# Optimization experiments

Hardware: AMD Instinct MI355X
Metric: run time of the kernel (lower is better)

The kernel has to match this reference:

```python
import jax, jax.numpy as jnp
import numpy as np
import math

B, S, D = 2, 4096, 512
H, DH = 8, 64
L = 128            # num_landmarks
W = 128            # window_size
EXT = W // 2       # 64
WIN = 2 * EXT + W  # 256
G = S // W         # 32 chunks
EPS = 1e-5


def _ln(x, g, b):
    mu = jnp.mean(x, axis=-1, keepdims=True)
    var = jnp.mean((x - mu) ** 2, axis=-1, keepdims=True)
    return (x - mu) * jax.lax.rsqrt(var + EPS) * g + b


def setup_inputs() -> dict:
    key = jax.random.key(0)
    ks = jax.random.split(key, 12)
    sd = 1.0 / math.sqrt(D)
    inp = {
        "X": jax.random.normal(ks[0], (B, S, D), dtype=jnp.float32),
        "mask": jnp.ones((B, S), dtype=jnp.int32),
        "Wq": jax.random.normal(ks[1], (D, H * DH), dtype=jnp.float32) * sd,
        "bq": jnp.zeros((H * DH,), jnp.float32),
        "Wk": jax.random.normal(ks[2], (D, H * DH), dtype=jnp.float32) * sd,
        "bk": jnp.zeros((H * DH,), jnp.float32),
        "Wv": jax.random.normal(ks[3], (D, H * DH), dtype=jnp.float32) * sd,
        "bv": jnp.zeros((H * DH,), jnp.float32),
        "Wo": jax.random.normal(ks[4], (H * DH, D), dtype=jnp.float32) * sd,
        "bo": jnp.zeros((D,), jnp.float32),
        "ln_l_g": jnp.ones((H * DH,), jnp.float32),
        "ln_l_b": jnp.zeros((H * DH,), jnp.float32),
        "ln_s_g": jnp.ones((H * DH,), jnp.float32),
        "ln_s_b": jnp.zeros((H * DH,), jnp.float32),
        "Wd": jax.random.normal(ks[5], (D, H * L), dtype=jnp.float32) * sd,
        "bd": jnp.zeros((H * L,), jnp.float32),
    }
    return inp


def reference(X, mask, Wq, bq, Wk, bk, Wv, bv, Wo, bo,
              ln_l_g, ln_l_b, ln_s_g, ln_s_b, Wd, bd):
    scale = 1.0 / math.sqrt(DH)

    def split(x):  # [B,S,H*DH] -> [B,H,S,DH]
        return x.reshape(B, S, H, DH).transpose(0, 2, 1, 3)

    Q = split(X @ Wq + bq) * scale
    K = split(_ln(X @ Wk + bk, ln_l_g, ln_l_b))
    V = split(_ln(X @ Wv + bv, ln_l_g, ln_l_b))
    pad_mask = (mask == 0)  # True = padding, [B,S]

    # ---- landmark compression branch ----
    hs = jax.nn.softmax((X @ Wd + bd).astype(jnp.float32), axis=1)  # over seq
    hs = hs.astype(X.dtype).reshape(B, S, H, L).transpose(0, 2, 3, 1)  # [B,H,L,S]
    Kc = jnp.einsum('bhls,bhsd->bhld', hs, K)
    Vc = jnp.einsum('bhls,bhsd->bhld', hs, V)
    # dual_ln_s over full model dim
    Kc = _ln(Kc.transpose(0, 2, 1, 3).reshape(B, L, H * DH), ln_s_g, ln_s_b)
    Kc = Kc.reshape(B, L, H, DH).transpose(0, 2, 1, 3)
    Vc = _ln(Vc.transpose(0, 2, 1, 3).reshape(B, L, H * DH), ln_s_g, ln_s_b)
    Vc = Vc.reshape(B, L, H, DH).transpose(0, 2, 1, 3)

    attn_c = jnp.einsum('bhqd,bhld->bhql', Q, Kc)  # [B,H,S,L]

    # ---- sliding-window branch (v2 tiling) ----
    idx = jnp.arange(G)[:, None] * W + jnp.arange(WIN)[None, :]
    K_pad = jnp.pad(K, ((0, 0), (0, 0), (EXT, EXT), (0, 0)))
    K_tiles = K_pad[:, :, idx, :]
    Qt = Q.reshape(B, H, G, W, DH)
    win_scores = jnp.einsum('bhgqd,bhgkd->bhgqk', Qt, K_tiles)
    mask_pad = jnp.pad(pad_mask, ((0, 0), (EXT, EXT)), constant_values=True)
    mask_tiles = mask_pad[:, idx]
    win_scores = jnp.where(mask_tiles[:, None, :, None, :], -jnp.inf, win_scores)
    win_scores = win_scores.reshape(B, H, S, WIN)

    # ---- joint softmax over [landmarks | window] ----
    all_scores = jnp.concatenate([attn_c, win_scores], axis=-1)
    all_attn = jax.nn.softmax(all_scores.astype(jnp.float32), axis=-1).astype(X.dtype)
    all_attn = jnp.where(pad_mask[:, None, :, None], 0.0, all_attn)

    C = jnp.einsum('bhql,bhld->bhqd', all_attn[..., :L], Vc)
    wp = all_attn[..., L:].reshape(B, H, G, W, WIN)
    V_pad = jnp.pad(V, ((0, 0), (0, 0), (EXT, EXT), (0, 0)))
    V_tiles = V_pad[:, :, idx, :]
    C = C + jnp.einsum('bhgqk,bhgkd->bhgqd', wp, V_tiles).reshape(B, H, S, DH)

    out = C.transpose(0, 2, 1, 3).reshape(B, S, H * DH) @ Wo + bo
    return out
```

## Files before the change

### kernel.cpp

```cpp
#include <hip/hip_runtime.h>
#include <hip/hip_bf16.h>

#define S_LEN 4096
#define Hn 8
#define DHn 64
#define Lc 128
#define HL 1024
#define KD 512

typedef __attribute__((ext_vector_type(8))) short bshort8;
typedef __attribute__((ext_vector_type(4))) float f32x4;

__device__ __forceinline__ short f2bs(float f) {
    union { float f; unsigned u; } x; x.f = f;
    const unsigned r = x.u + 0x7FFFu + ((x.u >> 16) & 1u);
    return (short)(r >> 16);
}
__device__ __forceinline__ float bs2f(short s) {
    union { unsigned u; float f; } x; x.u = ((unsigned)(unsigned short)s) << 16;
    return x.f;
}

__device__ __forceinline__ void gl16(const short* g, short* l) {
    __builtin_amdgcn_global_load_lds((const __attribute__((address_space(1))) void*)g,
                                     (__attribute__((address_space(3))) void*)l, 16, 0, 0);
}

__global__ __launch_bounds__(256) void prep_all(const float* __restrict__ X,
    const float* __restrict__ Wq, const float* __restrict__ Wk, const float* __restrict__ Wv,
    const float* __restrict__ Wd, const float* __restrict__ Wo,
    short* __restrict__ Xbf, short* __restrict__ WTall, short* __restrict__ WoT)
{
    const int t = threadIdx.x;
    int blk = blockIdx.x;
    if (blk < 2048) {
        const int i = (blk * 256 + t) * 8;
        const float4 a = *(const float4*)&X[i];
        const float4 b = *(const float4*)&X[i + 4];
        bshort8 o;
        o[0] = f2bs(a.x); o[1] = f2bs(a.y); o[2] = f2bs(a.z); o[3] = f2bs(a.w);
        o[4] = f2bs(b.x); o[5] = f2bs(b.y); o[6] = f2bs(b.z); o[7] = f2bs(b.w);
        *(bshort8*)&Xbf[i] = o;
        return;
    }
    blk -= 2048;
    const float* W; short* out; int N;
    if (blk < 256)       { W = Wq; out = WTall;              N = 512;  }
    else if (blk < 512)  { W = Wk; out = WTall + 512 * 512;  N = 512;  blk -= 256; }
    else if (blk < 768)  { W = Wv; out = WTall + 1024 * 512; N = 512;  blk -= 512; }
    else if (blk < 1280) { W = Wd; out = WTall + 1536 * 512; N = 1024; blk -= 768; }
    else                 { W = Wo; out = WoT;                N = 512;  blk -= 1280; }
    const int nb = N >> 5;
    const int n0 = (blk % nb) * 32, k0 = (blk / nb) * 32;
    __shared__ float Tl[32][33];
    const int tx = t & 31, ty = t >> 5;
#pragma unroll
    for (int i = ty; i < 32; i += 8)
        Tl[i][tx] = W[(size_t)(k0 + i) * N + n0 + tx];
    __syncthreads();
#pragma unroll
    for (int i = ty; i < 32; i += 8)
        out[(size_t)(n0 + i) * KD + k0 + tx] = f2bs(Tl[tx][i]);
}

__global__ __launch_bounds__(256) void gemm_proj(const short* __restrict__ Xbf,
    const short* __restrict__ WT,
    const float* __restrict__ bq, const float* __restrict__ bk,
    const float* __restrict__ bv, const float* __restrict__ bd,
    short* __restrict__ Qbf, short* __restrict__ KbBf, short* __restrict__ VbBf,
    short* __restrict__ DlogBf)
{
    __shared__ __align__(16) short A_s[128 * 64];
    __shared__ __align__(16) short B_s[128 * 64];
    const int t = threadIdx.x;
    const int n0 = blockIdx.x * 128, m0 = blockIdx.y * 128;
    const int lane = t & 63, wave = t >> 6;
    const int wm = wave >> 1, wn = wave & 1;
    const int quad = lane >> 4, r15 = lane & 15;
    const int srow = t >> 3, scol = (t & 7) * 8;
    f32x4 acc[4][4];
#pragma unroll
    for (int i = 0; i < 4; ++i)
#pragma unroll
        for (int j = 0; j < 4; ++j) acc[i][j] = (f32x4){0.f, 0.f, 0.f, 0.f};

    for (int kk = 0; kk < KD; kk += 64) {
#pragma unroll
        for (int r = 0; r < 4; ++r) {
            gl16(&Xbf[(size_t)(m0 + r * 32 + srow) * KD + kk + scol], &A_s[r * 2048 + t * 8]);
            gl16(&WT[(size_t)(n0 + r * 32 + srow) * KD + kk + scol],  &B_s[r * 2048 + t * 8]);
        }
        __syncthreads();
#pragma unroll
        for (int ks = 0; ks < 2; ++ks) {
            bshort8 af[4], bfr[4];
#pragma unroll
            for (int i = 0; i < 4; ++i) af[i]  = *(const bshort8*)&A_s[(wm * 64 + i * 16 + r15) * 64 + ks * 32 + quad * 8];
#pragma unroll
            for (int j = 0; j < 4; ++j) bfr[j] = *(const bshort8*)&B_s[(wn * 64 + j * 16 + r15) * 64 + ks * 32 + quad * 8];
#pragma unroll
            for (int i = 0; i < 4; ++i)
#pragma unroll
                for (int j = 0; j < 4; ++j)
                    acc[i][j] = __builtin_amdgcn_mfma_f32_16x16x32_bf16(af[i], bfr[j], acc[i][j], 0, 0, 0);
        }
        __syncthreads();
    }
    const int seg = (n0 >= 1536) ? 3 : (n0 >> 9);
#pragma unroll
    for (int i = 0; i < 4; ++i)
#pragma unroll
        for (int j = 0; j < 4; ++j)
#pragma unroll
            for (int r = 0; r < 4; ++r) {
                const int gm = m0 + wm * 64 + i * 16 + quad * 4 + r;
                const int gn = n0 + wn * 64 + j * 16 + r15;
                float v = acc[i][j][r];
                if (seg == 0) {
                    v = (v + bq[gn]) * 0.125f;
                    const int bb = gm >> 12, s = gm & 4095, hh = gn >> 6, d = gn & 63;
                    Qbf[((size_t)(bb * Hn + hh) * S_LEN + s) * DHn + d] = f2bs(v);
                } else if (seg == 1) {
                    KbBf[(size_t)gm * 512 + (gn - 512)] = f2bs(v + bk[gn - 512]);
                } else if (seg == 2) {
                    VbBf[(size_t)gm * 512 + (gn - 1024)] = f2bs(v + bv[gn - 1024]);
                } else {
                    DlogBf[(size_t)gm * 1024 + (gn - 1536)] = f2bs(v + bd[gn - 1536]);
                }
            }
}

__global__ __launch_bounds__(256) void gemm_out(const short* __restrict__ Abf,
    const short* __restrict__ WT, const float* __restrict__ bias, float* __restrict__ outp)
{
    __shared__ __align__(16) short A_s[64 * 32];
    __shared__ __align__(16) short B_s[64 * 32];
    const int t = threadIdx.x;
    const int n0 = blockIdx.x * 64, m0 = blockIdx.y * 64;
    const int lane = t & 63, wave = t >> 6;
    const int quad = lane >> 4, r15 = lane & 15;
    const int eOff = t * 8;
    const int am = eOff >> 5, ak = eOff & 31;
    f32x4 acc[4];
#pragma unroll
    for (int j = 0; j < 4; ++j) acc[j] = (f32x4){0.f, 0.f, 0.f, 0.f};

    for (int kk = 0; kk < KD; kk += 32) {
        gl16(&Abf[(size_t)(m0 + am) * KD + kk + ak], &A_s[eOff]);
        gl16(&WT[(size_t)(n0 + am) * KD + kk + ak],  &B_s[eOff]);
        __syncthreads();
        const bshort8 af = *(const bshort8*)&A_s[(wave * 16 + r15) * 32 + quad * 8];
#pragma unroll
        for (int j = 0; j < 4; ++j) {
            const bshort8 bfr = *(const bshort8*)&B_s[(j * 16 + r15) * 32 + quad * 8];
            acc[j] = __builtin_amdgcn_mfma_f32_16x16x32_bf16(af, bfr, acc[j], 0, 0, 0);
        }
        __syncthreads();
    }
#pragma unroll
    for (int j = 0; j < 4; ++j)
#pragma unroll
        for (int r = 0; r < 4; ++r) {
            const int gm = m0 + wave * 16 + quad * 4 + r;
            const int gn = n0 + j * 16 + r15;
            outp[(size_t)gm * 512 + gn] = acc[j][r] + bias[gn];
        }
}

__global__ __launch_bounds__(256) void ln_ip(const short* __restrict__ KbBf, const short* __restrict__ VbBf,
    const float* __restrict__ g, const float* __restrict__ beta,
    short* __restrict__ Kbf, short* __restrict__ Vbf)
{
    const short* src = blockIdx.y ? VbBf : KbBf;
    short* dst = blockIdx.y ? Vbf : Kbf;
    const int row = blockIdx.x, t = threadIdx.x;
    const size_t base = (size_t)row * 512;
    const float x0 = bs2f(src[base + t]);
    const float x1 = bs2f(src[base + t + 256]);
    float s = x0 + x1, ss = x0 * x0 + x1 * x1;
#pragma unroll
    for (int off = 32; off >= 1; off >>= 1) { s += __shfl_xor(s, off); ss += __shfl_xor(ss, off); }
    __shared__ float red[2][4];
    if ((t & 63) == 0) { red[0][t >> 6] = s; red[1][t >> 6] = ss; }
    __syncthreads();
    s = red[0][0] + red[0][1] + red[0][2] + red[0][3];
    ss = red[1][0] + red[1][1] + red[1][2] + red[1][3];
    const float mu = s * (1.f / 512.f);
    const float r = rsqrtf(ss * (1.f / 512.f) - mu * mu + 1e-5f);
    const int bb = row >> 12, sidx = row & 4095;
#pragma unroll
    for (int half = 0; half < 2; ++half) {
        const int c = t + half * 256;
        const float x = half ? x1 : x0;
        const float v = (x - mu) * r * g[c] + beta[c];
        dst[((size_t)(bb * Hn + (c >> 6)) * S_LEN + sidx) * DHn + (c & 63)] = f2bs(v);
    }
}

__global__ __launch_bounds__(256) void kcvc_mfma(const short* __restrict__ Dlog,
    const short* __restrict__ Kbf, const short* __restrict__ Vbf,
    short* __restrict__ partK, short* __restrict__ partV, float* __restrict__ partZ)
{
    __shared__ __align__(16) short aa[128 * 72];
    __shared__ __align__(16) short Kt[64 * 72];
    __shared__ __align__(16) short Vt[64 * 72];
    __shared__ float zsh[256];
    const int t = threadIdx.x;
    const int seg = blockIdx.x, h = blockIdx.y, b = blockIdx.z;
    const int s0 = seg * 128;
    const size_t bh = (size_t)(b * Hn + h);
    const int lane = t & 63, wave = t >> 6;
    const int quad = lane >> 4, r15 = lane & 15;
    const int al = t & 127, ah = t >> 7;
    const int vj = t & 63, vd0 = (t >> 6) * 16;
    float zacc = 0.f;
    f32x4 aK[2][4], aV[2][4];
#pragma unroll
    for (int i = 0; i < 2; ++i)
#pragma unroll
        for (int j = 0; j < 4; ++j) { aK[i][j] = (f32x4){0.f,0.f,0.f,0.f}; aV[i][j] = (f32x4){0.f,0.f,0.f,0.f}; }

    for (int c = 0; c < 2; ++c) {
        const int sc0 = s0 + c * 64;
        if (c) __syncthreads();
#pragma unroll
        for (int gch = 0; gch < 4; ++gch) {
            bshort8 o;
#pragma unroll
            for (int j = 0; j < 8; ++j) {
                const int s = sc0 + ah * 32 + gch * 8 + j;
                const float e = __expf(bs2f(Dlog[((size_t)b * S_LEN + s) * HL + h * Lc + al]));
                zacc += e;
                o[j] = f2bs(e);
            }
            *(bshort8*)&aa[al * 72 + ah * 32 + gch * 8] = o;
        }
        {
            const size_t rb = (bh * S_LEN + sc0 + vj) * DHn + vd0;
            const bshort8 k0 = *(const bshort8*)&Kbf[rb];
            const bshort8 k1 = *(const bshort8*)&Kbf[rb + 8];
            const bshort8 v0 = *(const bshort8*)&Vbf[rb];
            const bshort8 v1 = *(const bshort8*)&Vbf[rb + 8];
#pragma unroll
            for (int i = 0; i < 8; ++i) {
                Kt[(vd0 + i) * 72 + vj] = k0[i]; Kt[(vd0 + 8 + i) * 72 + vj] = k1[i];
                Vt[(vd0 + i) * 72 + vj] = v0[i]; Vt[(vd0 + 8 + i) * 72 + vj] = v1[i];
            }
        }
        __syncthreads();
#pragma unroll
        for (int ks = 0; ks < 2; ++ks) {
            const bshort8 a0 = *(const bshort8*)&aa[(wave * 32 + r15) * 72 + ks * 32 + quad * 8];
            const bshort8 a1 = *(const bshort8*)&aa[(wave * 32 + 16 + r15) * 72 + ks * 32 + quad * 8];
#pragma unroll
            for (int j = 0; j < 4; ++j) {
                const bshort8 bk = *(const bshort8*)&Kt[(j * 16 + r15) * 72 + ks * 32 + quad * 8];
                const bshort8 bv = *(const bshort8*)&Vt[(j * 16 + r15) * 72 + ks * 32 + quad * 8];
                aK[0][j] = __builtin_amdgcn_mfma_f32_16x16x32_bf16(a0, bk, aK[0][j], 0, 0, 0);
                aK[1][j] = __builtin_amdgcn_mfma_f32_16x16x32_bf16(a1, bk, aK[1][j], 0, 0, 0);
                aV[0][j] = __builtin_amdgcn_mfma_f32_16x16x32_bf16(a0, bv, aV[0][j], 0, 0, 0);
                aV[1][j] = __builtin_amdgcn_mfma_f32_16x16x32_bf16(a1, bv, aV[1][j], 0, 0, 0);
            }
        }
    }
    zsh[t] = zacc;
    __syncthreads();
    if (t < 128)
        partZ[((size_t)(bh * Lc + t)) * 32 + seg] = zsh[t] + zsh[t + 128];
#pragma unroll
    for (int i = 0; i < 2; ++i)
#pragma unroll
        for (int j = 0; j < 4; ++j)
#pragma unroll
            for (int r = 0; r < 4; ++r) {
                const int l = wave * 32 + i * 16 + quad * 4 + r;
                const int d = j * 16 + r15;
                const size_t o = (((size_t)(b * Lc + l)) * 32 + seg) * 512 + h * 64 + d;
                partK[o] = f2bs(aK[i][j][r]);
                partV[o] = f2bs(aV[i][j][r]);
            }
}

__global__ __launch_bounds__(256) void kcvc_s2(const short* __restrict__ partK,
    const short* __restrict__ partV, const float* __restrict__ partZ,
    const float* __restrict__ g, const float* __restrict__ beta,
    short* __restrict__ KcBf, short* __restrict__ VcBf)
{
    const int l = blockIdx.x, b = blockIdx.y, t = threadIdx.x;
    __shared__ float zh[8];
    if (t < 8) {
        float z = 0.f;
        const size_t zb = ((size_t)((b * Hn + t) * Lc + l)) * 32;
#pragma unroll
        for (int seg = 0; seg < 32; ++seg) z += partZ[zb + seg];
        zh[t] = 1.f / z;
    }
    const size_t base = ((size_t)(b * Lc + l)) * 32 * 512;
    float k0 = 0.f, k1 = 0.f, v0 = 0.f, v1 = 0.f;
    for (int ch = 0; ch < 32; ++ch) {
        const size_t o = base + (size_t)ch * 512;
        k0 += bs2f(partK[o + t]);       k1 += bs2f(partK[o + t + 256]);
        v0 += bs2f(partV[o + t]);       v1 += bs2f(partV[o + t + 256]);
    }
    __syncthreads();
    const float z0 = zh[t >> 6], z1 = zh[(t + 256) >> 6];
    k0 *= z0; k1 *= z1; v0 *= z0; v1 *= z1;
    float sk = k0 + k1, ssk = k0 * k0 + k1 * k1;
    float sv = v0 + v1, ssv = v0 * v0 + v1 * v1;
#pragma unroll
    for (int off = 32; off >= 1; off >>= 1) {
        sk += __shfl_xor(sk, off); ssk += __shfl_xor(ssk, off);
        sv += __shfl_xor(sv, off); ssv += __shfl_xor(ssv, off);
    }
    __shared__ float red[4][4];
    if ((t & 63) == 0) {
        red[0][t >> 6] = sk; red[1][t >> 6] = ssk;
        red[2][t >> 6] = sv; red[3][t >> 6] = ssv;
    }
    __syncthreads();
    sk = red[0][0] + red[0][1] + red[0][2] + red[0][3];
    ssk = red[1][0] + red[1][1] + red[1][2] + red[1][3];
    sv = red[2][0] + red[2][1] + red[2][2] + red[2][3];
    ssv = red[3][0] + red[3][1] + red[3][2] + red[3][3];
    const float muK = sk * (1.f / 512.f);
    const float rK = rsqrtf(ssk * (1.f / 512.f) - muK * muK + 1e-5f);
    const float muV = sv * (1.f / 512.f);
    const float rV = rsqrtf(ssv * (1.f / 512.f) - muV * muV + 1e-5f);
#pragma unroll
    for (int half = 0; half < 2; ++half) {
        const int c = t + half * 256;
        const float xk = half ? k1 : k0;
        const float xv = half ? v1 : v0;
        const size_t o = ((size_t)(b * Hn + (c >> 6)) * Lc + l) * DHn + (c & 63);
        KcBf[o] = f2bs((xk - muK) * rK * g[c] + beta[c]);
        VcBf[o] = f2bs((xv - muV) * rV * g[c] + beta[c]);
    }
}

__global__ __launch_bounds__(256) void attn_mfma(
    const short* __restrict__ Qbf, const short* __restrict__ Kbf, const short* __restrict__ Vbf,
    const short* __restrict__ KcBf, const short* __restrict__ VcBf,
    const int* __restrict__ mask, short* __restrict__ C)
{
    __shared__ __align__(16) short Q_l[64 * 72];
    __shared__ __align__(16) short K_l[64 * 72];
    __shared__ __align__(16) short Vt_l[64 * 72];
    __shared__ __align__(16) short P_l[64 * 72];
    __shared__ float vb[64];
    const int t = threadIdx.x;
    const int qt = blockIdx.x, h = blockIdx.y, b = blockIdx.z;
    const int q0 = qt * 64, gg = qt >> 1;
    const size_t bh = (size_t)(b * Hn + h);
    const int lane = t & 63, wave = t >> 6;
    const int quad = lane >> 4, r15 = lane & 15;
    const int sr = t >> 2, sc = (t & 3) * 16;
    const int vj = t & 63, vd0 = (t >> 6) * 16;

    {
        const size_t gq = (bh * S_LEN + q0 + sr) * DHn + sc;
        const bshort8 a = *(const bshort8*)&Qbf[gq];
        const bshort8 b8 = *(const bshort8*)&Qbf[gq + 8];
        *(bshort8*)&Q_l[sr * 72 + sc] = a;
        *(bshort8*)&Q_l[sr * 72 + sc + 8] = b8;
    }
    f32x4 o[4];
#pragma unroll
    for (int df = 0; df < 4; ++df) o[df] = (f32x4){0.f, 0.f, 0.f, 0.f};
    float lrow[4] = {0.f, 0.f, 0.f, 0.f};

    for (int cc = 0; cc < 6; ++cc) {
        const short* ksrc; const short* vsrc;
        int sk0 = 0;
        if (cc < 2) {
            ksrc = &KcBf[(bh * Lc + cc * 64) * DHn];
            vsrc = &VcBf[(bh * Lc + cc * 64) * DHn];
        } else {
            sk0 = gg * 128 - 64 + (cc - 2) * 64;
            if (sk0 < 0 || sk0 >= S_LEN) continue;
            ksrc = &Kbf[(bh * S_LEN + sk0) * DHn];
            vsrc = &Vbf[(bh * S_LEN + sk0) * DHn];
        }
        __syncthreads();
        if (t < 64) {
            float v = 0.f;
            if (cc >= 2 && mask[b * S_LEN + sk0 + t] == 0) v = -1e30f;
            vb[t] = v;
        }
        {
            const bshort8 a = *(const bshort8*)&ksrc[sr * 64 + sc];
            const bshort8 b8 = *(const bshort8*)&ksrc[sr * 64 + sc + 8];
            *(bshort8*)&K_l[sr * 72 + sc] = a;
            *(bshort8*)&K_l[sr * 72 + sc + 8] = b8;
        }
        {
            const bshort8 v0 = *(const bshort8*)&vsrc[vj * 64 + vd0];
            const bshort8 v1 = *(const bshort8*)&vsrc[vj * 64 + vd0 + 8];
#pragma unroll
            for (int i = 0; i < 8; ++i) {
                Vt_l[(vd0 + i) * 72 + vj] = v0[i];
                Vt_l[(vd0 + 8 + i) * 72 + vj] = v1[i];
            }
        }
        __syncthreads();
        f32x4 c[4];
#pragma unroll
        for (int jf = 0; jf < 4; ++jf) c[jf] = (f32x4){0.f, 0.f, 0.f, 0.f};
#pragma unroll
        for (int ks = 0; ks < 2; ++ks) {
            const bshort8 aq = *(const bshort8*)&Q_l[(wave * 16 + r15) * 72 + ks * 32 + quad * 8];
#pragma unroll
            for (int jf = 0; jf < 4; ++jf) {
                const bshort8 bk = *(const bshort8*)&K_l[(jf * 16 + r15) * 72 + ks * 32 + quad * 8];
                c[jf] = __builtin_amdgcn_mfma_f32_16x16x32_bf16(aq, bk, c[jf], 0, 0, 0);
            }
        }
        float vbl[4];
#pragma unroll
        for (int jf = 0; jf < 4; ++jf) vbl[jf] = vb[jf * 16 + r15];
        float sum[4] = {0.f, 0.f, 0.f, 0.f};
#pragma unroll
        for (int jf = 0; jf < 4; ++jf)
#pragma unroll
            for (int r = 0; r < 4; ++r) {
                const float p = __expf(c[jf][r] + vbl[jf]);
                sum[r] += p;
                P_l[(wave * 16 + quad * 4 + r) * 72 + jf * 16 + r15] = f2bs(p);
            }
#pragma unroll
        for (int off = 1; off <= 8; off <<= 1)
#pragma unroll
            for (int r = 0; r < 4; ++r) sum[r] += __shfl_xor(sum[r], off);
#pragma unroll
        for (int r = 0; r < 4; ++r) lrow[r] += sum[r];
#pragma unroll
        for (int ks = 0; ks < 2; ++ks) {
            const bshort8 ap = *(const bshort8*)&P_l[(wave * 16 + r15) * 72 + ks * 32 + quad * 8];
#pragma unroll
            for (int df = 0; df < 4; ++df) {
                const bshort8 bv = *(const bshort8*)&Vt_l[(df * 16 + r15) * 72 + ks * 32 + quad * 8];
                o[df] = __builtin_amdgcn_mfma_f32_16x16x32_bf16(ap, bv, o[df], 0, 0, 0);
            }
        }
    }
#pragma unroll
    for (int r = 0; r < 4; ++r) {
        const int q = q0 + wave * 16 + quad * 4 + r;
        const float rl = (mask[b * S_LEN + q] == 0) ? 0.f : (1.f / lrow[r]);
        const size_t ob = ((size_t)b * S_LEN + q) * 512 + h * 64;
#pragma unroll
        for (int df = 0; df < 4; ++df)
            C[ob + df * 16 + r15] = f2bs(o[df][r] * rl);
    }
}

extern "C" void kernel_launch(void* const* d_in, const int* in_sizes, int n_in,
                              void* d_out, int out_size, void* d_ws, size_t ws_size,
                              hipStream_t stream) {
    (void)in_sizes; (void)n_in; (void)out_size; (void)ws_size;
    const float* X    = (const float*)d_in[0];
    const int*   mask = (const int*)d_in[1];
    const float* Wq = (const float*)d_in[2];  const float* bq = (const float*)d_in[3];
    const float* Wk = (const float*)d_in[4];  const float* bk = (const float*)d_in[5];
    const float* Wv = (const float*)d_in[6];  const float* bv = (const float*)d_in[7];
    const float* Wo = (const float*)d_in[8];  const float* bo = (const float*)d_in[9];
    const float* lnlg = (const float*)d_in[10]; const float* lnlb = (const float*)d_in[11];
    const float* lnsg = (const float*)d_in[12]; const float* lnsb = (const float*)d_in[13];
    const float* Wd = (const float*)d_in[14]; const float* bd = (const float*)d_in[15];

    short* sw = (short*)d_ws;
    short* Qbf    = sw;
    short* Kbf    = Qbf + 4194304;
    short* Vbf    = Kbf + 4194304;
    short* KbBf   = Vbf + 4194304;
    short* VbBf   = KbBf + 4194304;
    short* DlogBf = VbBf + 4194304;
    short* Xbf    = DlogBf + 8388608;
    short* WTall  = Xbf + 4194304;
    short* WoT    = WTall + 1310720;
    short* KcBf   = WoT + 262144;
    short* VcBf   = KcBf + 131072;
    short* partV  = VcBf + 131072;
    float* partZ  = (float*)(partV + 4194304);
    short* partK  = Xbf;
    short* Cbf    = Xbf;

    const dim3 blk(256);
    prep_all<<<3584, blk, 0, stream>>>(X, Wq, Wk, Wv, Wd, Wo, Xbf, WTall, WoT);
    gemm_proj<<<dim3(20, 64), blk, 0, stream>>>(Xbf, WTall, bq, bk, bv, bd, Qbf, KbBf, VbBf, DlogBf);
    ln_ip<<<dim3(8192, 2), blk, 0, stream>>>(KbBf, VbBf, lnlg, lnlb, Kbf, Vbf);
    kcvc_mfma<<<dim3(32, 8, 2), blk, 0, stream>>>(DlogBf, Kbf, Vbf, partK, partV, partZ);
    kcvc_s2<<<dim3(128, 2), blk, 0, stream>>>(partK, partV, partZ, lnsg, lnsb, KcBf, VcBf);
    attn_mfma<<<dim3(64, 8, 2), blk, 0, stream>>>(Qbf, Kbf, Vbf, KcBf, VcBf, mask, Cbf);
    gemm_out<<<dim3(8, 128), blk, 0, stream>>>(Cbf, WoT, bo, (float*)d_out);
}
```

Baseline: 238.3 us.

## Double attention query tile to 128 rows and halve projection GEMM K-step

```diff
diff --git a/kernel.cpp b/kernel.cpp
--- a/kernel.cpp
+++ b/kernel.cpp
@@ -70,40 +70,37 @@
     short* __restrict__ Qbf, short* __restrict__ KbBf, short* __restrict__ VbBf,
     short* __restrict__ DlogBf)
 {
-    __shared__ __align__(16) short A_s[128 * 64];
-    __shared__ __align__(16) short B_s[128 * 64];
+    __shared__ __align__(16) short A_s[128 * 32];
+    __shared__ __align__(16) short B_s[128 * 32];
     const int t = threadIdx.x;
     const int n0 = blockIdx.x * 128, m0 = blockIdx.y * 128;
     const int lane = t & 63, wave = t >> 6;
     const int wm = wave >> 1, wn = wave & 1;
     const int quad = lane >> 4, r15 = lane & 15;
-    const int srow = t >> 3, scol = (t & 7) * 8;
+    const int eOff = t * 8;
+    const int am = eOff >> 5, ak = eOff & 31;
     f32x4 acc[4][4];
 #pragma unroll
     for (int i = 0; i < 4; ++i)
 #pragma unroll
         for (int j = 0; j < 4; ++j) acc[i][j] = (f32x4){0.f, 0.f, 0.f, 0.f};
 
-    for (int kk = 0; kk < KD; kk += 64) {
-#pragma unroll
-        for (int r = 0; r < 4; ++r) {
-            gl16(&Xbf[(size_t)(m0 + r * 32 + srow) * KD + kk + scol], &A_s[r * 2048 + t * 8]);
-            gl16(&WT[(size_t)(n0 + r * 32 + srow) * KD + kk + scol],  &B_s[r * 2048 + t * 8]);
-        }
-        __syncthreads();
-#pragma unroll
-        for (int ks = 0; ks < 2; ++ks) {
-            bshort8 af[4], bfr[4];
-#pragma unroll
-            for (int i = 0; i < 4; ++i) af[i]  = *(const bshort8*)&A_s[(wm * 64 + i * 16 + r15) * 64 + ks * 32 + quad * 8];
-#pragma unroll
-            for (int j = 0; j < 4; ++j) bfr[j] = *(const bshort8*)&B_s[(wn * 64 + j * 16 + r15) * 64 + ks * 32 + quad * 8];
-#pragma unroll
-            for (int i = 0; i < 4; ++i)
-#pragma unroll
-                for (int j = 0; j < 4; ++j)
-                    acc[i][j] = __builtin_amdgcn_mfma_f32_16x16x32_bf16(af[i], bfr[j], acc[i][j], 0, 0, 0);
-        }
+    for (int kk = 0; kk < KD; kk += 32) {
+        gl16(&Xbf[(size_t)(m0 + am) * KD + kk + ak],      &A_s[eOff]);
+        gl16(&Xbf[(size_t)(m0 + 64 + am) * KD + kk + ak], &A_s[2048 + eOff]);
+        gl16(&WT[(size_t)(n0 + am) * KD + kk + ak],       &B_s[eOff]);
+        gl16(&WT[(size_t)(n0 + 64 + am) * KD + kk + ak],  &B_s[2048 + eOff]);
+        __syncthreads();
+        bshort8 af[4], bfr[4];
+#pragma unroll
+        for (int i = 0; i < 4; ++i) af[i]  = *(const bshort8*)&A_s[(wm * 64 + i * 16 + r15) * 32 + quad * 8];
+#pragma unroll
+        for (int j = 0; j < 4; ++j) bfr[j] = *(const bshort8*)&B_s[(wn * 64 + j * 16 + r15) * 32 + quad * 8];
+#pragma unroll
+        for (int i = 0; i < 4; ++i)
+#pragma unroll
+            for (int j = 0; j < 4; ++j)
+                acc[i][j] = __builtin_amdgcn_mfma_f32_16x16x32_bf16(af[i], bfr[j], acc[i][j], 0, 0, 0);
         __syncthreads();
     }
     const int seg = (n0 >= 1536) ? 3 : (n0 >> 9);
@@ -342,31 +339,35 @@
     const short* __restrict__ KcBf, const short* __restrict__ VcBf,
     const int* __restrict__ mask, short* __restrict__ C)
 {
-    __shared__ __align__(16) short Q_l[64 * 72];
+    __shared__ __align__(16) short Q_l[128 * 72];
     __shared__ __align__(16) short K_l[64 * 72];
     __shared__ __align__(16) short Vt_l[64 * 72];
-    __shared__ __align__(16) short P_l[64 * 72];
+    __shared__ __align__(16) short P_l[128 * 72];
     __shared__ float vb[64];
     const int t = threadIdx.x;
     const int qt = blockIdx.x, h = blockIdx.y, b = blockIdx.z;
-    const int q0 = qt * 64, gg = qt >> 1;
+    const int q0 = qt * 128;
     const size_t bh = (size_t)(b * Hn + h);
     const int lane = t & 63, wave = t >> 6;
     const int quad = lane >> 4, r15 = lane & 15;
     const int sr = t >> 2, sc = (t & 3) * 16;
     const int vj = t & 63, vd0 = (t >> 6) * 16;
 
-    {
-        const size_t gq = (bh * S_LEN + q0 + sr) * DHn + sc;
+#pragma unroll
+    for (int r = 0; r < 2; ++r) {
+        const int row = r * 64 + sr;
+        const size_t gq = (bh * S_LEN + q0 + row) * DHn + sc;
         const bshort8 a = *(const bshort8*)&Qbf[gq];
         const bshort8 b8 = *(const bshort8*)&Qbf[gq + 8];
-        *(bshort8*)&Q_l[sr * 72 + sc] = a;
-        *(bshort8*)&Q_l[sr * 72 + sc + 8] = b8;
-    }
-    f32x4 o[4];
-#pragma unroll
-    for (int df = 0; df < 4; ++df) o[df] = (f32x4){0.f, 0.f, 0.f, 0.f};
-    float lrow[4] = {0.f, 0.f, 0.f, 0.f};
+        *(bshort8*)&Q_l[row * 72 + sc] = a;
+        *(bshort8*)&Q_l[row * 72 + sc + 8] = b8;
+    }
+    f32x4 o[2][4];
+#pragma unroll
+    for (int i = 0; i < 2; ++i)
+#pragma unroll
+        for (int df = 0; df < 4; ++df) o[i][df] = (f32x4){0.f, 0.f, 0.f, 0.f};
+    float lrow[2][4] = {{0.f, 0.f, 0.f, 0.f}, {0.f, 0.f, 0.f, 0.f}};
 
     for (int cc = 0; cc < 6; ++cc) {
         const short* ksrc; const short* vsrc;
@@ -375,7 +376,7 @@
             ksrc = &KcBf[(bh * Lc + cc * 64) * DHn];
             vsrc = &VcBf[(bh * Lc + cc * 64) * DHn];
         } else {
-            sk0 = gg * 128 - 64 + (cc - 2) * 64;
+            sk0 = q0 - 64 + (cc - 2) * 64;
             if (sk0 < 0 || sk0 >= S_LEN) continue;
             ksrc = &Kbf[(bh * S_LEN + sk0) * DHn];
             vsrc = &Vbf[(bh * S_LEN + sk0) * DHn];
@@ -402,55 +403,73 @@
             }
         }
         __syncthreads();
-        f32x4 c[4];
-#pragma unroll
-        for (int jf = 0; jf < 4; ++jf) c[jf] = (f32x4){0.f, 0.f, 0.f, 0.f};
+        f32x4 c[2][4];
+#pragma unroll
+        for (int i = 0; i < 2; ++i)
+#pragma unroll
+            for (int jf = 0; jf < 4; ++jf) c[i][jf] = (f32x4){0.f, 0.f, 0.f, 0.f};
 #pragma unroll
         for (int ks = 0; ks < 2; ++ks) {
-            const bshort8 aq = *(const bshort8*)&Q_l[(wave * 16 + r15) * 72 + ks * 32 + quad * 8];
+            bshort8 aq[2];
+#pragma unroll
+            for (int i = 0; i < 2; ++i)
+                aq[i] = *(const bshort8*)&Q_l[(wave * 32 + i * 16 + r15) * 72 + ks * 32 + quad * 8];
 #pragma unroll
             for (int jf = 0; jf < 4; ++jf) {
                 const bshort8 bk = *(const bshort8*)&K_l[(jf * 16 + r15) * 72 + ks * 32 + quad * 8];
-                c[jf] = __builtin_amdgcn_mfma_f32_16x16x32_bf16(aq, bk, c[jf], 0, 0, 0);
+                c[0][jf] = __builtin_amdgcn_mfma_f32_16x16x32_bf16(aq[0], bk, c[0][jf], 0, 0, 0);
+                c[1][jf] = __builtin_amdgcn_mfma_f32_16x16x32_bf16(aq[1], bk, c[1][jf], 0, 0, 0);
             }
         }
         float vbl[4];
 #pragma unroll
         for (int jf = 0; jf < 4; ++jf) vbl[jf] = vb[jf * 16 + r15];
-        float sum[4] = {0.f, 0.f, 0.f, 0.f};
-#pragma unroll
-        for (int jf = 0; jf < 4; ++jf)
-#pragma unroll
-            for (int r = 0; r < 4; ++r) {
-                const float p = __expf(c[jf][r] + vbl[jf]);
-                sum[r] += p;
-                P_l[(wave * 16 + quad * 4 + r) * 72 + jf * 16 + r15] = f2bs(p);
-            }
+        float sum[2][4] = {{0.f, 0.f, 0.f, 0.f}, {0.f, 0.f, 0.f, 0.f}};
+#pragma unroll
+        for (int i = 0; i < 2; ++i)
+#pragma unroll
+            for (int jf = 0; jf < 4; ++jf)
+#pragma unroll
+                for (int r = 0; r < 4; ++r) {
+                    const float p = __expf(c[i][jf][r] + vbl[jf]);
+                    sum[i][r] += p;
+                    P_l[(wave * 32 + i * 16 + quad * 4 + r) * 72 + jf * 16 + r15] = f2bs(p);
+                }
 #pragma unroll
         for (int off = 1; off <= 8; off <<= 1)
 #pragma unroll
-            for (int r = 0; r < 4; ++r) sum[r] += __shfl_xor(sum[r], off);
-#pragma unroll
-        for (int r = 0; r < 4; ++r) lrow[r] += sum[r];
+            for (int i = 0; i < 2; ++i)
+#pragma unroll
+                for (int r = 0; r < 4; ++r) sum[i][r] += __shfl_xor(sum[i][r], off);
+#pragma unroll
+        for (int i = 0; i < 2; ++i)
+#pragma unroll
+            for (int r = 0; r < 4; ++r) lrow[i][r] += sum[i][r];
 #pragma unroll
         for (int ks = 0; ks < 2; ++ks) {
-            const bshort8 ap = *(const bshort8*)&P_l[(wave * 16 + r15) * 72 + ks * 32 + quad * 8];
+            bshort8 ap[2];
+#pragma unroll
+            for (int i = 0; i < 2; ++i)
+                ap[i] = *(const bshort8*)&P_l[(wave * 32 + i * 16 + r15) * 72 + ks * 32 + quad * 8];
 #pragma unroll
             for (int df = 0; df < 4; ++df) {
                 const bshort8 bv = *(const bshort8*)&Vt_l[(df * 16 + r15) * 72 + ks * 32 + quad * 8];
-                o[df] = __builtin_amdgcn_mfma_f32_16x16x32_bf16(ap, bv, o[df], 0, 0, 0);
-            }
-        }
-    }
-#pragma unroll
-    for (int r = 0; r < 4; ++r) {
-        const int q = q0 + wave * 16 + quad * 4 + r;
-        const float rl = (mask[b * S_LEN + q] == 0) ? 0.f : (1.f / lrow[r]);
-        const size_t ob = ((size_t)b * S_LEN + q) * 512 + h * 64;
-#pragma unroll
-        for (int df = 0; df < 4; ++df)
-            C[ob + df * 16 + r15] = f2bs(o[df][r] * rl);
-    }
+                o[0][df] = __builtin_amdgcn_mfma_f32_16x16x32_bf16(ap[0], bv, o[0][df], 0, 0, 0);
+                o[1][df] = __builtin_amdgcn_mfma_f32_16x16x32_bf16(ap[1], bv, o[1][df], 0, 0, 0);
+            }
+        }
+    }
+#pragma unroll
+    for (int i = 0; i < 2; ++i)
+#pragma unroll
+        for (int r = 0; r < 4; ++r) {
+            const int q = q0 + wave * 32 + i * 16 + quad * 4 + r;
+            const float rl = (mask[b * S_LEN + q] == 0) ? 0.f : (1.f / lrow[i][r]);
+            const size_t ob = ((size_t)b * S_LEN + q) * 512 + h * 64;
+#pragma unroll
+            for (int df = 0; df < 4; ++df)
+                C[ob + df * 16 + r15] = f2bs(o[i][df][r] * rl);
+        }
 }
 
 extern "C" void kernel_launch(void* const* d_in, const int* in_sizes, int n_in,
@@ -490,6 +509,6 @@
     ln_ip<<<dim3(8192, 2), blk, 0, stream>>>(KbBf, VbBf, lnlg, lnlb, Kbf, Vbf);
     kcvc_mfma<<<dim3(32, 8, 2), blk, 0, stream>>>(DlogBf, Kbf, Vbf, partK, partV, partZ);
     kcvc_s2<<<dim3(128, 2), blk, 0, stream>>>(partK, partV, partZ, lnsg, lnsb, KcBf, VcBf);
-    attn_mfma<<<dim3(64, 8, 2), blk, 0, stream>>>(Qbf, Kbf, Vbf, KcBf, VcBf, mask, Cbf);
+    attn_mfma<<<dim3(32, 8, 2), blk, 0, stream>>>(Qbf, Kbf, Vbf, KcBf, VcBf, mask, Cbf);
     gemm_out<<<dim3(8, 128), blk, 0, stream>>>(Cbf, WoT, bo, (float*)d_out);
 }
```

Result: faster. 220.9 us (-7.3%).
